# Performance work log

Hardware: AMD Instinct MI355X
Metric: run time of the kernel (lower is better)

Reference implementation:

```python
import jax, jax.numpy as jnp
import numpy as np

D_MODEL = 1024
N_HEADS = 16
HEAD_DIM = D_MODEL // N_HEADS
EPS = 1e-6


def setup_inputs() -> dict:
    key = jax.random.key(0)
    k1, k2, k3 = jax.random.split(key, 3)
    b, l, d = 2, 2048, D_MODEL
    x = jax.random.normal(k1, (b, l, d), dtype=jnp.float32)
    # Linear weights stored so that y = x @ W (no bias), matching torch math
    w_qkv = jax.random.normal(k2, (d, 3 * d), dtype=jnp.float32) * (1.0 / np.sqrt(d))
    w_proj = jax.random.normal(k3, (d, d), dtype=jnp.float32) * (1.0 / np.sqrt(d))
    norm_w = jnp.ones((d,), dtype=jnp.float32)
    return {"x": x, "norm_w": norm_w, "w_qkv": w_qkv, "w_proj": w_proj}


def rms_norm(x, w, eps=EPS):
    x32 = x.astype(jnp.float32)
    inv_rms = jax.lax.rsqrt(jnp.mean(x32 * x32, axis=-1, keepdims=True) + eps)
    return (x32 * inv_rms).astype(x.dtype) * w.astype(x.dtype)


def reference(x, norm_w, w_qkv, w_proj):
    b, l, d = x.shape
    h = rms_norm(x, norm_w)
    qkv = h @ w_qkv                       # [b, l, 3d]
    q, k, v = jnp.split(qkv, 3, axis=-1)

    def heads(t):
        return t.reshape(b, l, N_HEADS, HEAD_DIM).transpose(0, 2, 1, 3)  # [b,h,l,hd]

    q, k, v = heads(q), heads(k), heads(v)
    scale = 1.0 / np.sqrt(HEAD_DIM)
    scores = jnp.einsum('bhqd,bhkd->bhqk', q, k) * scale  # full LxL scores
    attn = jax.nn.softmax(scores, axis=-1)
    ctx = jnp.einsum('bhqk,bhkd->bhqd', attn, v)
    ctx = ctx.transpose(0, 2, 1, 3).reshape(b, l, d)
    out = ctx @ w_proj
    return x + out
```

## Files before the change

### kernel.cpp

```cpp
#include <hip/hip_runtime.h>
#include <hip/hip_bf16.h>
#include <cstdint>
#include <cstddef>

typedef __attribute__((ext_vector_type(8))) short bf16x8;
typedef __attribute__((ext_vector_type(4))) float f32x4;
typedef __attribute__((ext_vector_type(16))) float f32x16;

#define GLD_LDS16(gptr, lptr)                                                  \
  __builtin_amdgcn_global_load_lds(                                            \
      (const __attribute__((address_space(1))) void*)(gptr),                   \
      (__attribute__((address_space(3))) void*)(lptr), 16, 0, 0)

__device__ __forceinline__ uint32_t cvtpk(float a, float b) {
  uint32_t d;
  asm("v_cvt_pk_bf16_f32 %0, %1, %2" : "=v"(d) : "v"(a), "v"(b));
  return d;
}

__device__ __forceinline__ float xhalf_sum(float x) {
  auto r = __builtin_amdgcn_permlane32_swap(__float_as_uint(x),
                                            __float_as_uint(x), false, false);
  return __uint_as_float(r[0]) + __uint_as_float(r[1]);
}

__global__ __launch_bounds__(256) void rmsnorm_kernel(
    const float* __restrict__ x, const float* __restrict__ w,
    __hip_bfloat16* __restrict__ h) {
  const int row = blockIdx.x;
  const int tid = threadIdx.x;
  const float4 v = reinterpret_cast<const float4*>(x + (size_t)row * 1024)[tid];
  float ss = v.x * v.x + v.y * v.y + v.z * v.z + v.w * v.w;
#pragma unroll
  for (int off = 32; off >= 1; off >>= 1) ss += __shfl_down(ss, off);
  __shared__ float red[4];
  if ((tid & 63) == 0) red[tid >> 6] = ss;
  __syncthreads();
  const float inv =
      rsqrtf((red[0] + red[1] + red[2] + red[3]) * (1.0f / 1024.0f) + 1e-6f);
  const float4 wv = reinterpret_cast<const float4*>(w)[tid];
  __hip_bfloat16* hp = h + (size_t)row * 1024 + tid * 4;
  hp[0] = __float2bfloat16(v.x * inv * wv.x);
  hp[1] = __float2bfloat16(v.y * inv * wv.y);
  hp[2] = __float2bfloat16(v.z * inv * wv.z);
  hp[3] = __float2bfloat16(v.w * inv * wv.w);
}

__global__ __launch_bounds__(256) void transpose_cast2_kernel(
    const float* __restrict__ w_qkv, const float* __restrict__ w_proj,
    __hip_bfloat16* __restrict__ wqkvT, __hip_bfloat16* __restrict__ wprojT) {
  __shared__ float tile[32][33];
  const float* src;
  __hip_bfloat16* dst;
  int C, bx;
  if (blockIdx.x < 96) {
    src = w_qkv; dst = wqkvT; C = 3072; bx = blockIdx.x * 32;
  } else {
    src = w_proj; dst = wprojT; C = 1024; bx = (blockIdx.x - 96) * 32;
  }
  const int R = 1024;
  const int by = blockIdx.y * 32;
  const int tx = threadIdx.x;
  const int ty = threadIdx.y;
#pragma unroll
  for (int j = 0; j < 32; j += 8)
    tile[ty + j][tx] = src[(size_t)(by + ty + j) * C + bx + tx];
  __syncthreads();
#pragma unroll
  for (int j = 0; j < 32; j += 8)
    dst[(size_t)(bx + ty + j) * R + by + tx] = __float2bfloat16(tile[tx][ty + j]);
}

template <int BM, int BN, int RESID>
__device__ __forceinline__ void gemm_tile(
    const __hip_bfloat16* __restrict__ A, const __hip_bfloat16* __restrict__ BT,
    void* __restrict__ Cout, const float* __restrict__ resid, int M, int N,
    int K, int bx, int by, __hip_bfloat16* As, __hip_bfloat16* Bs) {
  const int tid = threadIdx.x;
  const int lane = tid & 63;
  const int wid = tid >> 6;
  const int m0 = by * BM;
  const int n0 = bx * BN;
  const int wr = wid >> 1, wc = wid & 1;
  constexpr int MI = BM / 32, NJ = BN / 32;
  constexpr int NCHA = BM / 16, NCHB = BN / 16;
  f32x4 acc[MI][NJ] = {};
  const int nk = K >> 5;
  const int lr = lane & 15, lk = lane >> 4;
  for (int kt = 0; kt < nk; ++kt) {
#pragma unroll
    for (int it = 0; it < NCHA / 4; ++it) {
      const int c = wid + it * 4;
      const int e = c * 512 + lane * 8;
      GLD_LDS16(A + (size_t)(m0 + (e >> 5)) * K + kt * 32 + (e & 31),
                As + c * 512);
    }
#pragma unroll
    for (int it = 0; it < NCHB / 4; ++it) {
      const int c = wid + it * 4;
      const int e = c * 512 + lane * 8;
      GLD_LDS16(BT + (size_t)(n0 + (e >> 5)) * K + kt * 32 + (e & 31),
                Bs + c * 512);
    }
    __syncthreads();
    bf16x8 af[MI], bfr[NJ];
#pragma unroll
    for (int i = 0; i < MI; ++i)
      af[i] = *(const bf16x8*)(As + (wr * (BM / 2) + i * 16 + lr) * 32 + lk * 8);
#pragma unroll
    for (int j = 0; j < NJ; ++j)
      bfr[j] = *(const bf16x8*)(Bs + (wc * (BN / 2) + j * 16 + lr) * 32 + lk * 8);
#pragma unroll
    for (int i = 0; i < MI; ++i)
#pragma unroll
      for (int j = 0; j < NJ; ++j)
        acc[i][j] = __builtin_amdgcn_mfma_f32_16x16x32_bf16(af[i], bfr[j],
                                                            acc[i][j], 0, 0, 0);
    __syncthreads();
  }
#pragma unroll
  for (int i = 0; i < MI; ++i)
#pragma unroll
    for (int j = 0; j < NJ; ++j)
#pragma unroll
      for (int r = 0; r < 4; ++r) {
        const int row = m0 + wr * (BM / 2) + i * 16 + lk * 4 + r;
        const int col = n0 + wc * (BN / 2) + j * 16 + lr;
        const float v = acc[i][j][r];
        if (RESID) {
          ((float*)Cout)[(size_t)row * N + col] =
              resid[(size_t)row * N + col] + v;
        } else {
          ((__hip_bfloat16*)Cout)[(size_t)row * N + col] = __float2bfloat16(v);
        }
      }
}

__global__ __launch_bounds__(256) void qkv_gemm_kernel(
    const __hip_bfloat16* __restrict__ h, const __hip_bfloat16* __restrict__ wqkT,
    const __hip_bfloat16* __restrict__ wvT, __hip_bfloat16* __restrict__ qkbuf,
    __hip_bfloat16* __restrict__ vTbuf) {
  __shared__ __align__(16) __hip_bfloat16 As[128 * 32];
  __shared__ __align__(16) __hip_bfloat16 Bs[128 * 32];
  const int bid = blockIdx.x;
  if (bid < 512) {
    const int xcd = bid & 7, seq = bid >> 3;
    const int by = (xcd >> 1) * 8 + (seq >> 3);
    const int bx = (xcd & 1) * 8 + (seq & 7);
    gemm_tile<128, 128, 0>(h, wqkT, (void*)qkbuf, nullptr, 4096, 2048, 1024,
                           bx, by, As, Bs);
  } else {
    const int t = bid - 512;
    const int xcd = t & 7, seq = t >> 3;
    const int by = seq >> 2;
    const int bx = xcd * 4 + (seq & 3);
    gemm_tile<128, 128, 0>(wvT, h, (void*)vTbuf, nullptr, 1024, 4096, 1024, bx,
                           by, As, Bs);
  }
}

__global__ __launch_bounds__(256) void proj_gemm_kernel(
    const __hip_bfloat16* __restrict__ ctx, const __hip_bfloat16* __restrict__ wpT,
    float* __restrict__ out, const float* __restrict__ x) {
  __shared__ __align__(16) __hip_bfloat16 As[128 * 32];
  __shared__ __align__(16) __hip_bfloat16 Bs[64 * 32];
  const int bid = blockIdx.x;
  const int xcd = bid & 7, seq = bid >> 3;
  const int by = xcd * 4 + (seq >> 4);
  const int bx = seq & 15;
  gemm_tile<128, 64, 1>(ctx, wpT, (void*)out, x, 4096, 1024, 1024, bx, by, As,
                        Bs);
}

__global__ __launch_bounds__(256, 2) void attn_kernel(
    const __hip_bfloat16* __restrict__ qk, const __hip_bfloat16* __restrict__ vT,
    __hip_bfloat16* __restrict__ ctx) {
  const int flat = blockIdx.x;
  const int xcd = flat & 7, seq = flat >> 3;
  const int bh = xcd * 4 + (seq >> 4);
  const int qt = seq & 15;
  const int b = bh >> 4, h = bh & 15;
  const int tid = threadIdx.x, lane = tid & 63, wid = tid >> 6;
  const size_t tok0 = (size_t)b * 2048;
  const int q0 = qt * 128 + wid * 32;
  const int l31 = lane & 31;
  const int hi = lane >> 5;

  __shared__ __align__(16) char Kl[3][64 * 128];
  __shared__ __align__(16) char Vl[3][64 * 128];

  const int sr = tid >> 2;
  const int scB = (tid & 3) * 32;
  const int swW = (sr & 7) << 4;
  const int wA = sr * 128 + (scB ^ swW);
  const int wB = sr * 128 + ((scB + 16) ^ swW);

  const __hip_bfloat16* kbase = qk + tok0 * 2048 + 1024 + (size_t)h * 64;
  const __hip_bfloat16* vbase = vT + ((size_t)(h * 64 + sr)) * 4096 + tok0;
  const int scE = (tid & 3) * 16;

  bf16x8 qf[4];
  {
    const __hip_bfloat16* qptr = qk + (tok0 + q0 + l31) * 2048 + h * 64 + hi * 8;
    const float c = 0.125f * 1.44269504f;
#pragma unroll
    for (int ks = 0; ks < 4; ++ks) {
      bf16x8 v = *(const bf16x8*)(qptr + ks * 16);
      const __hip_bfloat16* ie = (const __hip_bfloat16*)&v;
      __hip_bfloat16* oe = (__hip_bfloat16*)&qf[ks];
#pragma unroll
      for (int i = 0; i < 8; ++i)
        oe[i] = __float2bfloat16(__bfloat162float(ie[i]) * c);
    }
  }

  const int swR = (l31 & 7) << 4;
  const int rb0 = l31 * 128;
  const int rb1 = (32 + l31) * 128;

  bf16x8 kreg0, kreg1, vreg0, vreg1;
  auto load_tile = [&](int t) {
    const __hip_bfloat16* kp = kbase + (size_t)(t * 64 + sr) * 2048 + scE;
    kreg0 = *(const bf16x8*)kp;
    kreg1 = *(const bf16x8*)(kp + 8);
    const __hip_bfloat16* vp = vbase + t * 64 + scE;
    vreg0 = *(const bf16x8*)vp;
    vreg1 = *(const bf16x8*)(vp + 8);
  };
  auto write_tile = [&](int bf) {
    *(bf16x8*)(Kl[bf] + wA) = kreg0;
    *(bf16x8*)(Kl[bf] + wB) = kreg1;
    *(bf16x8*)(Vl[bf] + wA) = vreg0;
    *(bf16x8*)(Vl[bf] + wB) = vreg1;
  };
  auto qk_tile = [&](int bf, f32x16& d0, f32x16& d1) {
#pragma unroll
    for (int ks = 0; ks < 4; ++ks) {
      const int cOff = (ks * 32 + hi * 16) ^ swR;
      const bf16x8 kf0 = *(const bf16x8*)(Kl[bf] + rb0 + cOff);
      const bf16x8 kf1 = *(const bf16x8*)(Kl[bf] + rb1 + cOff);
      d0 = __builtin_amdgcn_mfma_f32_32x32x16_bf16(kf0, qf[ks], d0, 0, 0, 0);
      d1 = __builtin_amdgcn_mfma_f32_32x32x16_bf16(kf1, qf[ks], d1, 0, 0, 0);
    }
  };

  f32x16 oT0 = {}, oT1 = {};
  float lacc = 0.f;

  load_tile(0);
  write_tile(0);
  load_tile(1);
  __syncthreads();
  f32x16 s0 = {}, s1 = {};
  qk_tile(0, s0, s1);

  int bcur = 0, bnext = 1, bnn = 2;
  for (int t = 0; t < 32; ++t) {
    float ps = 0.f;
    uint32_t pk0[8], pk1[8];
#pragma unroll
    for (int i = 0; i < 8; ++i) {
      const float a0 = __builtin_amdgcn_exp2f(s0[2 * i]);
      const float a1 = __builtin_amdgcn_exp2f(s0[2 * i + 1]);
      const float b0 = __builtin_amdgcn_exp2f(s1[2 * i]);
      const float b1 = __builtin_amdgcn_exp2f(s1[2 * i + 1]);
      ps += (a0 + a1) + (b0 + b1);
      pk0[i] = cvtpk(a0, a1);
      pk1[i] = cvtpk(b0, b1);
    }
    lacc += ps;

    if (t + 1 < 32) write_tile(bnext);
    if (t + 2 < 32) load_tile(t + 2);
    __syncthreads();

    __builtin_amdgcn_s_setprio(1);
    f32x16 ns0 = {}, ns1 = {};
    if (t + 1 < 32) qk_tile(bnext, ns0, ns1);

#pragma unroll
    for (int ts = 0; ts < 4; ++ts) {
      const uint32_t* pk = (ts < 2) ? pk0 : pk1;
      const int o = (ts & 1) * 4;
      auto w02 = __builtin_amdgcn_permlane32_swap(pk[o], pk[o + 2], false, false);
      auto w13 =
          __builtin_amdgcn_permlane32_swap(pk[o + 1], pk[o + 3], false, false);
      uint32_t fr[4] = {w02[0], w13[0], w02[1], w13[1]};
      const bf16x8 pf = *(const bf16x8*)fr;
      const int cOff = (ts * 32 + hi * 16) ^ swR;
      const bf16x8 vf0 = *(const bf16x8*)(Vl[bcur] + rb0 + cOff);
      const bf16x8 vf1 = *(const bf16x8*)(Vl[bcur] + rb1 + cOff);
      oT0 = __builtin_amdgcn_mfma_f32_32x32x16_bf16(vf0, pf, oT0, 0, 0, 0);
      oT1 = __builtin_amdgcn_mfma_f32_32x32x16_bf16(vf1, pf, oT1, 0, 0, 0);
    }
    __builtin_amdgcn_s_setprio(0);

    s0 = ns0;
    s1 = ns1;
    const int tmp = bcur;
    bcur = bnext;
    bnext = bnn;
    bnn = tmp;
  }

  const float lrow = xhalf_sum(lacc);
  const float linv = 1.0f / lrow;
  __hip_bfloat16* cb = ctx + (tok0 + q0 + l31) * 1024 + h * 64;
#pragma unroll
  for (int dh = 0; dh < 2; ++dh) {
#pragma unroll
    for (int rq = 0; rq < 4; ++rq) {
      const int d0 = 8 * rq + 4 * hi + 32 * dh;
      float v0, v1, v2, v3;
      if (dh) {
        v0 = oT1[4 * rq];
        v1 = oT1[4 * rq + 1];
        v2 = oT1[4 * rq + 2];
        v3 = oT1[4 * rq + 3];
      } else {
        v0 = oT0[4 * rq];
        v1 = oT0[4 * rq + 1];
        v2 = oT0[4 * rq + 2];
        v3 = oT0[4 * rq + 3];
      }
      *(uint32_t*)(cb + d0) = cvtpk(v0 * linv, v1 * linv);
      *(uint32_t*)(cb + d0 + 2) = cvtpk(v2 * linv, v3 * linv);
    }
  }
}

extern "C" void kernel_launch(void* const* d_in, const int* in_sizes, int n_in,
                              void* d_out, int out_size, void* d_ws,
                              size_t ws_size, hipStream_t stream) {
  const float* x = (const float*)d_in[0];
  const float* norm_w = (const float*)d_in[1];
  const float* w_qkv = (const float*)d_in[2];
  const float* w_proj = (const float*)d_in[3];
  float* out = (float*)d_out;

  char* ws = (char*)d_ws;
  __hip_bfloat16* hbuf = (__hip_bfloat16*)(ws);
  __hip_bfloat16* wqkvT = (__hip_bfloat16*)(ws + (size_t)8 * 1024 * 1024);
  __hip_bfloat16* wprojT = (__hip_bfloat16*)(ws + (size_t)14 * 1024 * 1024);
  __hip_bfloat16* qkbuf = (__hip_bfloat16*)(ws + (size_t)16 * 1024 * 1024);
  __hip_bfloat16* vTbuf = (__hip_bfloat16*)(ws + (size_t)32 * 1024 * 1024);
  __hip_bfloat16* ctx = (__hip_bfloat16*)(ws + (size_t)40 * 1024 * 1024);

  rmsnorm_kernel<<<dim3(4096), dim3(256), 0, stream>>>(x, norm_w, hbuf);
  transpose_cast2_kernel<<<dim3(128, 32), dim3(32, 8), 0, stream>>>(
      w_qkv, w_proj, wqkvT, wprojT);
  qkv_gemm_kernel<<<dim3(768), dim3(256), 0, stream>>>(
      hbuf, wqkvT, wqkvT + (size_t)2048 * 1024, qkbuf, vTbuf);
  attn_kernel<<<dim3(512), dim3(256), 0, stream>>>(qkbuf, vTbuf, ctx);
  proj_gemm_kernel<<<dim3(512), dim3(256), 0, stream>>>(ctx, wprojT, out, x);
}
```

Measured before the change: 110.0 us.

## Stage K/V tiles via direct global-to-LDS loads and move the barrier

Replaces the register-staged K/V tile path (global load into VGPRs, then ds_write into a swizzled layout) with global_load_lds DMA straight into the triple-buffered LDS tiles. The XOR swizzle is now applied on the global address side, and each wave stages two 8-row chunks. Tile t+2 is issued at the top of each iteration and a single barrier sits at the end of the iteration. This is meant to cut VGPR use and LDS-write instructions and to overlap loads with compute. The risk is that the barrier's wait on outstanding vector memory may also stall on the just-issued prefetch, which would shorten the overlap.

After: 110.3 us. Within noise of the previous version (+0.2%).

```diff
diff --git a/kernel.cpp b/kernel.cpp
--- a/kernel.cpp
+++ b/kernel.cpp
@@ -189,15 +189,10 @@
   __shared__ __align__(16) char Kl[3][64 * 128];
   __shared__ __align__(16) char Vl[3][64 * 128];
 
-  const int sr = tid >> 2;
-  const int scB = (tid & 3) * 32;
-  const int swW = (sr & 7) << 4;
-  const int wA = sr * 128 + (scB ^ swW);
-  const int wB = sr * 128 + ((scB + 16) ^ swW);
-
-  const __hip_bfloat16* kbase = qk + tok0 * 2048 + 1024 + (size_t)h * 64;
-  const __hip_bfloat16* vbase = vT + ((size_t)(h * 64 + sr)) * 4096 + tok0;
-  const int scE = (tid & 3) * 16;
+  const int srowL = lane >> 3;
+  const int colE = ((lane & 7) ^ srowL) << 3;
+  const __hip_bfloat16* kbase0 = qk + tok0 * 2048 + 1024 + (size_t)h * 64;
+  const __hip_bfloat16* vbase0 = vT + (size_t)h * 64 * 4096 + tok0;
 
   bf16x8 qf[4];
   {
@@ -218,20 +213,15 @@
   const int rb0 = l31 * 128;
   const int rb1 = (32 + l31) * 128;
 
-  bf16x8 kreg0, kreg1, vreg0, vreg1;
-  auto load_tile = [&](int t) {
-    const __hip_bfloat16* kp = kbase + (size_t)(t * 64 + sr) * 2048 + scE;
-    kreg0 = *(const bf16x8*)kp;
-    kreg1 = *(const bf16x8*)(kp + 8);
-    const __hip_bfloat16* vp = vbase + t * 64 + scE;
-    vreg0 = *(const bf16x8*)vp;
-    vreg1 = *(const bf16x8*)(vp + 8);
-  };
-  auto write_tile = [&](int bf) {
-    *(bf16x8*)(Kl[bf] + wA) = kreg0;
-    *(bf16x8*)(Kl[bf] + wB) = kreg1;
-    *(bf16x8*)(Vl[bf] + wA) = vreg0;
-    *(bf16x8*)(Vl[bf] + wB) = vreg1;
+  auto stage_tile = [&](int bf, int t) {
+#pragma unroll
+    for (int i = 0; i < 2; ++i) {
+      const int c = wid * 2 + i;
+      const int tokr = t * 64 + c * 8 + srowL;
+      GLD_LDS16(kbase0 + (size_t)tokr * 2048 + colE, Kl[bf] + c * 1024);
+      GLD_LDS16(vbase0 + (size_t)(c * 8 + srowL) * 4096 + t * 64 + colE,
+                Vl[bf] + c * 1024);
+    }
   };
   auto qk_tile = [&](int bf, f32x16& d0, f32x16& d1) {
 #pragma unroll
@@ -247,15 +237,16 @@
   f32x16 oT0 = {}, oT1 = {};
   float lacc = 0.f;
 
-  load_tile(0);
-  write_tile(0);
-  load_tile(1);
+  stage_tile(0, 0);
+  stage_tile(1, 1);
   __syncthreads();
   f32x16 s0 = {}, s1 = {};
   qk_tile(0, s0, s1);
 
   int bcur = 0, bnext = 1, bnn = 2;
   for (int t = 0; t < 32; ++t) {
+    if (t + 2 < 32) stage_tile(bnn, t + 2);
+
     float ps = 0.f;
     uint32_t pk0[8], pk1[8];
 #pragma unroll
@@ -269,10 +260,6 @@
       pk1[i] = cvtpk(b0, b1);
     }
     lacc += ps;
-
-    if (t + 1 < 32) write_tile(bnext);
-    if (t + 2 < 32) load_tile(t + 2);
-    __syncthreads();
 
     __builtin_amdgcn_s_setprio(1);
     f32x16 ns0 = {}, ns1 = {};
@@ -294,6 +281,8 @@
       oT1 = __builtin_amdgcn_mfma_f32_32x32x16_bf16(vf1, pf, oT1, 0, 0, 0);
     }
     __builtin_amdgcn_s_setprio(0);
+
+    __syncthreads();
 
     s0 = ns0;
     s1 = ns1;
```
